# Performance work log

Hardware: AMD Instinct MI355X
Metric: run time of the kernel (lower is better)

The kernel has to match this reference:

```python
import jax, jax.numpy as jnp
import numpy as np

B, S, F_IN, D, DFF, MEM, L, H = 32, 512, 64, 512, 2048, 1024, 3, 8
K_NEIGH = 3
TEMP = 1.0


def _pos_encoding(s, d):
    pos = np.arange(s, dtype=np.float64)[:, None]
    div = np.exp(np.arange(0, d, 2, dtype=np.float64) * (-np.log(10000.0) / d))
    pe = np.zeros((s, d), np.float32)
    pe[:, 0::2] = np.sin(pos * div)
    pe[:, 1::2] = np.cos(pos * div)
    return jnp.asarray(pe)


def _ln(x, g, b, eps=1e-5):
    m = x.mean(-1, keepdims=True)
    v = ((x - m) ** 2).mean(-1, keepdims=True)
    return (x - m) * jax.lax.rsqrt(v + eps) * g + b


def _mha(x, qkv_w, qkv_b, out_w, out_b):
    b, s, d = x.shape
    dh = d // H
    qkv = x @ qkv_w.T + qkv_b                      # (b,s,3d)
    q, k, v = jnp.split(qkv, 3, axis=-1)
    rs = lambda t: t.reshape(b, s, H, dh).transpose(0, 2, 1, 3)   # (b,h,s,dh)
    q, k, v = rs(q), rs(k), rs(v)
    scores = jnp.einsum('bhqd,bhkd->bhqk', q, k) / np.sqrt(dh).astype(np.float32)
    att = jax.nn.softmax(scores, axis=-1)
    o = jnp.einsum('bhqk,bhkd->bhqd', att, v).transpose(0, 2, 1, 3).reshape(b, s, d)
    return o @ out_w.T + out_b


def _construct_graph(x):
    # x: (B, S, F) -> adjacency (B, F, F) via kNN on rank-1 similarity (as in source)
    f = x.mean(axis=1)                                   # (B,F)
    n = jnp.linalg.norm(f, axis=1, keepdims=True)
    fn = f / jnp.maximum(n, 1e-12)                       # F.normalize over full vector
    sim = jnp.einsum('bi,bj->bij', fn, fn)               # (B,F,F)
    nf = f.shape[1]
    k = min(K_NEIGH, nf - 1)
    _, idx = jax.lax.top_k(sim, k + 1)                   # (B,F,k+1)
    idx = idx[..., 1:]                                   # drop top-1 (self under source's assumption)
    bidx = jnp.arange(f.shape[0])[:, None, None]
    ridx = jnp.arange(nf)[None, :, None]
    A = jnp.zeros((f.shape[0], nf, nf), x.dtype).at[bidx, ridx, idx].set(1.0)
    A = jnp.maximum(A, jnp.swapaxes(A, 1, 2))            # symmetrize
    di = jnp.arange(nf)
    return A.at[:, di, di].set(1.0)                      # fill_diagonal_(1)


def _gcn(x, A, w1, b1, w2, b2):
    deg = A.sum(2, keepdims=True)
    An = A / jnp.where(deg == 0, jnp.ones_like(deg), deg)
    xt = jnp.swapaxes(x, 1, 2)                           # (B,F,S)
    h = jax.nn.relu(jnp.einsum('bfg,bgh->bfh', An, xt @ w1.T + b1))
    h = jnp.einsum('bfg,bgh->bfh', An, h @ w2.T + b2)
    return jnp.swapaxes(h, 1, 2)                         # (B,S,F)


def _metg_forward(x, W_in, b_in, qkv_w, qkv_b, out_w, out_b, ln1_g, ln1_b,
                  ln2_g, ln2_b, ff1_w, ff1_b, ff2_w, ff2_b, memory,
                  fc1_w, fc1_b, fc2_w, fc2_b, gc1_w, gc1_b, gc2_w, gc2_b):
    # transformer branch
    h = x @ W_in.T + b_in                                # (B,S,D)
    h = h + _pos_encoding(h.shape[1], h.shape[2])
    for l in range(L):  # post-norm TransformerEncoderLayer, relu FFN, dropout=eval
        h = _ln(h + _mha(h, qkv_w[l], qkv_b[l], out_w[l], out_b[l]), ln1_g[l], ln1_b[l])
        ff = jax.nn.relu(h @ ff1_w[l].T + ff1_b[l]) @ ff2_w[l].T + ff2_b[l]
        h = _ln(h + ff, ln2_g[l], ln2_b[l])
    # memory module
    sims = (h @ memory.T) / TEMP                         # (B,S,MEM)
    attn = jax.nn.softmax(sims, axis=-1)
    upd = attn @ memory                                  # (B,S,D)
    # decoder
    cat = jnp.concatenate([h, upd], axis=-1)             # (B,S,2D)
    t_out = jax.nn.relu(cat @ fc1_w.T + fc1_b) @ fc2_w.T + fc2_b
    # GCN branch
    A = _construct_graph(x)
    g_out = _gcn(x, A, gc1_w, gc1_b, gc2_w, gc2_b)
    return t_out, g_out, attn


def setup_inputs() -> dict:
    key = jax.random.key(0)
    ks = jax.random.split(key, 12)
    w = lambda k, shape, s=0.02: jax.random.normal(k, shape, jnp.float32) * s
    return {
        'x': jax.random.normal(ks[0], (B, S, F_IN), jnp.float32),
        'W_in': w(ks[1], (D, F_IN)), 'b_in': jnp.zeros((D,), jnp.float32),
        'qkv_w': w(ks[2], (L, 3 * D, D)), 'qkv_b': jnp.zeros((L, 3 * D), jnp.float32),
        'out_w': w(ks[3], (L, D, D)), 'out_b': jnp.zeros((L, D), jnp.float32),
        'ln1_g': jnp.ones((L, D), jnp.float32), 'ln1_b': jnp.zeros((L, D), jnp.float32),
        'ln2_g': jnp.ones((L, D), jnp.float32), 'ln2_b': jnp.zeros((L, D), jnp.float32),
        'ff1_w': w(ks[4], (L, DFF, D)), 'ff1_b': jnp.zeros((L, DFF), jnp.float32),
        'ff2_w': w(ks[5], (L, D, DFF)), 'ff2_b': jnp.zeros((L, D), jnp.float32),
        'memory': w(ks[6], (MEM, D), 0.05),
        'fc1_w': w(ks[7], (D, 2 * D)), 'fc1_b': jnp.zeros((D,), jnp.float32),
        'fc2_w': w(ks[8], (F_IN, D)), 'fc2_b': jnp.zeros((F_IN,), jnp.float32),
        'gc1_w': w(ks[9], (D, S)), 'gc1_b': jnp.zeros((D,), jnp.float32),
        'gc2_w': w(ks[10], (S, D)), 'gc2_b': jnp.zeros((S,), jnp.float32),
    }


def reference(x, W_in, b_in, qkv_w, qkv_b, out_w, out_b, ln1_g, ln1_b,
              ln2_g, ln2_b, ff1_w, ff1_b, ff2_w, ff2_b, memory,
              fc1_w, fc1_b, fc2_w, fc2_b, gc1_w, gc1_b, gc2_w, gc2_b):
    return _metg_forward(x, W_in, b_in, qkv_w, qkv_b, out_w, out_b, ln1_g, ln1_b,
                         ln2_g, ln2_b, ff1_w, ff1_b, ff2_w, ff2_b, memory,
                         fc1_w, fc1_b, fc2_w, fc2_b, gc1_w, gc1_b, gc2_w, gc2_b)
```

## Files before the change

### kernel.cpp

```cpp
#include <hip/hip_runtime.h>
#include <hip/hip_bf16.h>
#include <math.h>


namespace {

typedef unsigned short ushort_t;
using bf16x8 = __attribute__((ext_vector_type(8))) __bf16;
using f32x4 = __attribute__((ext_vector_type(4))) float;
using ushort8 = __attribute__((ext_vector_type(8))) unsigned short;

constexpr int Mrows = 32 * 512;

__device__ __forceinline__ unsigned short f2bf(float f) {
  unsigned int u = __builtin_bit_cast(unsigned int, f);
  u += 0x7fffu + ((u >> 16) & 1u);
  return (unsigned short)(u >> 16);
}
__device__ __forceinline__ float bf2f(ushort_t u) {
  unsigned int v = ((unsigned int)u) << 16;
  return __builtin_bit_cast(float, v);
}

__device__ __forceinline__ void g2lds16(const void* g, void* l) {
  __builtin_amdgcn_global_load_lds(
      (const __attribute__((address_space(1))) unsigned int*)g,
      (__attribute__((address_space(3))) unsigned int*)l, 16, 0, 0);
}

template <bool RELU, bool BF16OUT>
__global__ __launch_bounds__(256) void gemm_bf16(const ushort_t* __restrict__ A,
                                                 const ushort_t* __restrict__ B,
                                                 const float* __restrict__ bias,
                                                 void* __restrict__ Cv,
                                                 int M, int N, int K,
                                                 int lda, int ldc) {
  __shared__ __align__(16) ushort_t As[128 * 64];
  __shared__ __align__(16) ushort_t Bs[128 * 64];
  const int t = threadIdx.x;
  const int w = t >> 6, l = t & 63;
  const int m0 = blockIdx.x << 7, n0 = blockIdx.y << 7;
  const int srow = w * 32 + (l >> 3);
  const int scol = ((l & 7) ^ (l >> 3)) << 3;
  const ushort_t* agp = A + (size_t)(m0 + srow) * lda + scol;
  const ushort_t* bgp = B + (size_t)(n0 + srow) * K + scol;
  ushort_t* alds = &As[(w * 32) * 64];
  ushort_t* blds = &Bs[(w * 32) * 64];
  const int wr = w >> 1, wc = w & 1;
  const int lr = l & 15, g = l >> 4;
  const int sw = (l & 7) << 4;
  f32x4 acc[4][4] = {};
  for (int kt = 0; kt < K; kt += 64) {
    __syncthreads();
#pragma unroll
    for (int i = 0; i < 4; ++i) {
      g2lds16(agp + (size_t)(i * 8) * lda + kt, alds + i * 8 * 64);
      g2lds16(bgp + (size_t)(i * 8) * K + kt, blds + i * 8 * 64);
    }
    __syncthreads();
#pragma unroll
    for (int ki = 0; ki < 2; ++ki) {
      bf16x8 af[4], bf[4];
      const int kb = (ki * 64 + g * 16) ^ sw;
#pragma unroll
      for (int mi = 0; mi < 4; ++mi)
        af[mi] = *(const bf16x8*)((const char*)As + (wr * 64 + mi * 16 + lr) * 128 + kb);
#pragma unroll
      for (int ni = 0; ni < 4; ++ni)
        bf[ni] = *(const bf16x8*)((const char*)Bs + (wc * 64 + ni * 16 + lr) * 128 + kb);
#pragma unroll
      for (int mi = 0; mi < 4; ++mi)
#pragma unroll
        for (int ni = 0; ni < 4; ++ni)
          acc[mi][ni] = __builtin_amdgcn_mfma_f32_16x16x32_bf16(af[mi], bf[ni],
                                                                acc[mi][ni], 0, 0, 0);
    }
  }
  float bb[4];
#pragma unroll
  for (int ni = 0; ni < 4; ++ni)
    bb[ni] = bias ? bias[n0 + wc * 64 + ni * 16 + lr] : 0.f;
  const int crow0 = m0 + wr * 64 + g * 4;
  const int ccol0 = n0 + wc * 64 + lr;
  if (!BF16OUT) {
    float* Cf = (float*)Cv;
#pragma unroll
    for (int mi = 0; mi < 4; ++mi)
#pragma unroll
      for (int ni = 0; ni < 4; ++ni)
#pragma unroll
        for (int v = 0; v < 4; ++v) {
          float val = acc[mi][ni][v] + bb[ni];
          if (RELU) val = fmaxf(val, 0.f);
          Cf[(size_t)(crow0 + mi * 16 + v) * ldc + ccol0 + ni * 16] = val;
        }
  } else {
    ushort_t* Cb = (ushort_t*)Cv;
#pragma unroll
    for (int mi = 0; mi < 4; ++mi)
#pragma unroll
      for (int ni = 0; ni < 4; ++ni)
#pragma unroll
        for (int v = 0; v < 4; ++v) {
          float val = acc[mi][ni][v] + bb[ni];
          if (RELU) val = fmaxf(val, 0.f);
          Cb[(size_t)(crow0 + mi * 16 + v) * ldc + ccol0 + ni * 16] = f2bf(val);
        }
  }
}

__global__ __launch_bounds__(256) void flash_attn_mfma(const ushort_t* __restrict__ qkvb,
                                                       ushort_t* __restrict__ ctxb) {
  __shared__ __align__(16) ushort_t Qs[64 * 64];
  __shared__ __align__(16) ushort_t Ks[64 * 64];
  __shared__ __align__(16) ushort_t VT[64 * 64];
  __shared__ __align__(16) ushort_t Ps[64 * 64];
  const int qb = blockIdx.x, hh = blockIdx.y, b = blockIdx.z;
  const int t = threadIdx.x, w = t >> 6, l = t & 63;
  const int g = l >> 4, lr = l & 15, l7 = l & 7;
  const ushort_t* qkv0 = qkvb + (size_t)b * 512 * 1536 + hh * 64;
  {
    const int r8 = l >> 3;
    const int gcol = (l7 ^ r8) << 3;
#pragma unroll
    for (int i = 0; i < 2; ++i) {
      const int row = w * 16 + i * 8 + r8;
      g2lds16(qkv0 + (size_t)(qb * 64 + row) * 1536 + gcol, &Qs[(w * 16 + i * 8) * 64]);
    }
  }
  float mst = -INFINITY, lst = 0.f;
  f32x4 oacc[4] = {};
  const int vk0 = (t & 31) * 2;
  const int vdh0 = (t >> 5) * 8;
  for (int kt = 0; kt < 8; ++kt) {
    __syncthreads();
    {
      const int r8 = l >> 3;
      const int gcol = (l7 ^ r8) << 3;
#pragma unroll
      for (int i = 0; i < 2; ++i) {
        const int row = w * 16 + i * 8 + r8;
        g2lds16(qkv0 + 512 + (size_t)(kt * 64 + row) * 1536 + gcol,
                &Ks[(w * 16 + i * 8) * 64]);
      }
    }
    {
      const ushort_t* vp = qkv0 + 1024 + (size_t)(kt * 64 + vk0) * 1536 + vdh0;
      ushort8 v0 = *(const ushort8*)vp;
      ushort8 v1 = *(const ushort8*)(vp + 1536);
      const int slotbase = vk0 >> 3;
      const int inb = (vk0 & 7) * 2;
#pragma unroll
      for (int e = 0; e < 8; ++e) {
        const int dh = vdh0 + e;
        unsigned int word = (unsigned int)v0[e] | ((unsigned int)v1[e] << 16);
        *(unsigned int*)((char*)VT + dh * 128 + (((slotbase ^ (dh & 7)) << 4) + inb)) = word;
      }
    }
    __syncthreads();
    f32x4 sacc[4] = {};
#pragma unroll
// ... 26 lines not shown
      for (int v = 0; v < 4; ++v) {
        p[mi][v] = __expf(p[mi][v] - mnew);
        csum += p[mi][v];
      }
    csum += __shfl_xor(csum, 16);
    csum += __shfl_xor(csum, 32);
    lst = lst * al + csum;
    mst = mnew;
#pragma unroll
    for (int mi = 0; mi < 4; ++mi) oacc[mi] *= al;
    {
      char* pbase = (char*)Ps + (w * 16 + lr) * 128;
#pragma unroll
      for (int mi = 0; mi < 4; ++mi)
#pragma unroll
        for (int vp2 = 0; vp2 < 2; ++vp2) {
          const int klo = mi * 16 + g * 4 + vp2 * 2;
          unsigned int word = (unsigned int)f2bf(p[mi][vp2 * 2]) |
                              ((unsigned int)f2bf(p[mi][vp2 * 2 + 1]) << 16);
          *(unsigned int*)(pbase + (((klo >> 3) ^ l7) << 4) + (klo & 7) * 2) = word;
        }
    }
#pragma unroll
    for (int ki = 0; ki < 2; ++ki) {
      const int sb = ((ki * 4 + g) ^ l7) << 4;
      bf16x8 pf = *(const bf16x8*)((const char*)Ps + (w * 16 + lr) * 128 + sb);
#pragma unroll
      for (int mi = 0; mi < 4; ++mi) {
        bf16x8 vf = *(const bf16x8*)((const char*)VT + (mi * 16 + lr) * 128 + sb);
        oacc[mi] = __builtin_amdgcn_mfma_f32_16x16x32_bf16(vf, pf, oacc[mi], 0, 0, 0);
      }
    }
  }
  const float inv = 1.f / lst;
  ushort_t* op = ctxb + (size_t)(b * 512 + qb * 64 + w * 16 + lr) * 512 + hh * 64;
#pragma unroll
  for (int mi = 0; mi < 4; ++mi)
#pragma unroll
    for (int vp2 = 0; vp2 < 2; ++vp2) {
      const int dh = mi * 16 + g * 4 + vp2 * 2;
      unsigned int word = (unsigned int)f2bf(oacc[mi][vp2 * 2] * inv) |
                          ((unsigned int)f2bf(oacc[mi][vp2 * 2 + 1] * inv) << 16);
      *(unsigned int*)(op + dh) = word;
    }
}

#define OUTER16(ACC, A4, B4) do { \
  ACC[0][0] += (A4).x*(B4).x; ACC[0][1] += (A4).x*(B4).y; ACC[0][2] += (A4).x*(B4).z; ACC[0][3] += (A4).x*(B4).w; \
  ACC[1][0] += (A4).y*(B4).x; ACC[1][1] += (A4).y*(B4).y; ACC[1][2] += (A4).y*(B4).z; ACC[1][3] += (A4).y*(B4).w; \
  ACC[2][0] += (A4).z*(B4).x; ACC[2][1] += (A4).z*(B4).y; ACC[2][2] += (A4).z*(B4).z; ACC[2][3] += (A4).z*(B4).w; \
  ACC[3][0] += (A4).w*(B4).x; ACC[3][1] += (A4).w*(B4).y; ACC[3][2] += (A4).w*(B4).z; ACC[3][3] += (A4).w*(B4).w; \
} while (0)

template <bool BT, bool RELU, bool PE>
__global__ __launch_bounds__(256) void gemm64(const float* __restrict__ A,
                                              const float* __restrict__ Bm,
                                              const float* __restrict__ bias,
                                              float* __restrict__ C,
                                              int M, int N, int K,
                                              const float* __restrict__ peb,
                                              ushort_t* __restrict__ hbb) {
  __shared__ float As[16][68];
  __shared__ float Bs[16][68];
  const int t = threadIdx.x;
  const int m0 = blockIdx.x << 6;
  const int n0 = blockIdx.y << 6;
  const int r0 = (t >> 4) << 2;
  const int c0 = (t & 15) << 2;
  const int lm = t >> 2;
  const int lk4 = (t & 3) << 2;
  const int lkk = t >> 4;
  const int ln = (t & 15) << 2;
  float acc[4][4] = {{0.f, 0.f, 0.f, 0.f}, {0.f, 0.f, 0.f, 0.f},
                     {0.f, 0.f, 0.f, 0.f}, {0.f, 0.f, 0.f, 0.f}};
  for (int kt = 0; kt < K; kt += 16) {
    __syncthreads();
    float4 av = *reinterpret_cast<const float4*>(A + (size_t)(m0 + lm) * K + kt + lk4);
    As[lk4 + 0][lm] = av.x; As[lk4 + 1][lm] = av.y;
    As[lk4 + 2][lm] = av.z; As[lk4 + 3][lm] = av.w;
    if (BT) {
      float4 bv = *reinterpret_cast<const float4*>(Bm + (size_t)(n0 + lm) * K + kt + lk4);
      Bs[lk4 + 0][lm] = bv.x; Bs[lk4 + 1][lm] = bv.y;
      Bs[lk4 + 2][lm] = bv.z; Bs[lk4 + 3][lm] = bv.w;
    } else {
      float4 bv = *reinterpret_cast<const float4*>(Bm + (size_t)(kt + lkk) * N + n0 + ln);
      *reinterpret_cast<float4*>(&Bs[lkk][ln]) = bv;
    }
    __syncthreads();
#pragma unroll
    for (int k = 0; k < 16; ++k) {
      float4 a4 = *reinterpret_cast<const float4*>(&As[k][r0]);
      float4 b4 = *reinterpret_cast<const float4*>(&Bs[k][c0]);
      OUTER16(acc, a4, b4);
    }
  }
  float bb0 = 0.f, bb1 = 0.f, bb2 = 0.f, bb3 = 0.f;
  if (bias) {
    bb0 = bias[n0 + c0 + 0]; bb1 = bias[n0 + c0 + 1];
    bb2 = bias[n0 + c0 + 2]; bb3 = bias[n0 + c0 + 3];
  }
#pragma unroll
  for (int i = 0; i < 4; ++i) {
    float4 o;
    o.x = acc[i][0] + bb0; o.y = acc[i][1] + bb1;
    o.z = acc[i][2] + bb2; o.w = acc[i][3] + bb3;
    if (RELU) {
      o.x = fmaxf(o.x, 0.f); o.y = fmaxf(o.y, 0.f);
      o.z = fmaxf(o.z, 0.f); o.w = fmaxf(o.w, 0.f);
    }
    const int row = m0 + r0 + i;
    if (PE) {
      float4 p = *reinterpret_cast<const float4*>(peb + (size_t)(row & 511) * 512 + n0 + c0);
      o.x += p.x; o.y += p.y; o.z += p.z; o.w += p.w;
      ushort4 ob;
      ob.x = f2bf(o.x); ob.y = f2bf(o.y); ob.z = f2bf(o.z); ob.w = f2bf(o.w);
      *reinterpret_cast<ushort4*>(hbb + (size_t)row * 512 + n0 + c0) = ob;
    }
    *reinterpret_cast<float4*>(C + (size_t)row * N + n0 + c0) = o;
  }
}

__device__ __forceinline__ float bsum256(float v, float* red) {
#pragma unroll
  for (int off = 32; off; off >>= 1) v += __shfl_down(v, off);
  __syncthreads();
  if ((threadIdx.x & 63) == 0) red[threadIdx.x >> 6] = v;
  __syncthreads();
  return red[0] + red[1] + red[2] + red[3];
}

__device__ __forceinline__ float bmax256(float v, float* red) {
#pragma unroll
  for (int off = 32; off; off >>= 1) v = fmaxf(v, __shfl_down(v, off));
  __syncthreads();
  if ((threadIdx.x & 63) == 0) red[threadIdx.x >> 6] = v;
  __syncthreads();
  return fmaxf(fmaxf(red[0], red[1]), fmaxf(red[2], red[3]));
}

__global__ __launch_bounds__(256) void ln_fused(float* __restrict__ h,
                                                ushort_t* __restrict__ hbo,
                                                int hbs,
                                                const ushort_t* __restrict__ resb,
                                                const float* __restrict__ g,
                                                const float* __restrict__ bt) {
  __shared__ float red[4];
  const size_t row = blockIdx.x;
  float* hp = h + row * 512;
  ushort_t* hbp = hbo + row * hbs;
  const ushort_t* rp = resb + row * 512;
  const int t = threadIdx.x;
  float x0 = hp[t] + bf2f(rp[t]);
  float x1 = hp[t + 256] + bf2f(rp[t + 256]);
  float mean = bsum256(x0 + x1, red) * (1.f / 512.f);
  float d0 = x0 - mean, d1 = x1 - mean;
  float var = bsum256(d0 * d0 + d1 * d1, red) * (1.f / 512.f);
  float rstd = rsqrtf(var + 1e-5f);
  float y0 = d0 * rstd * g[t] + bt[t];
  float y1 = d1 * rstd * g[t + 256] + bt[t + 256];
  hp[t] = y0; hp[t + 256] = y1;
  hbp[t] = f2bf(y0); hbp[t + 256] = f2bf(y1);
}

__global__ __launch_bounds__(256) void softmax1024_cvt(float* __restrict__ p,
                                                       ushort_t* __restrict__ pb) {
  __shared__ float red[4];
  float4* rp = reinterpret_cast<float4*>(p + (size_t)blockIdx.x * 1024);
  ushort4* rb = reinterpret_cast<ushort4*>(pb + (size_t)blockIdx.x * 1024);
  const int t = threadIdx.x;
  float4 v = rp[t];
  float mx = bmax256(fmaxf(fmaxf(v.x, v.y), fmaxf(v.z, v.w)), red);
  float e0 = expf(v.x - mx), e1 = expf(v.y - mx), e2 = expf(v.z - mx), e3 = expf(v.w - mx);
  float sm = bsum256(e0 + e1 + e2 + e3, red);
  float inv = 1.f / sm;
  float4 o = make_float4(e0 * inv, e1 * inv, e2 * inv, e3 * inv);
  rp[t] = o;
  ushort4 ob;
  ob.x = f2bf(o.x); ob.y = f2bf(o.y); ob.z = f2bf(o.z); ob.w = f2bf(o.w);
  rb[t] = ob;
}

__global__ void pe_kernel(float* __restrict__ pe) {
  const int s = blockIdx.x, i = threadIdx.x;
  double div = exp((double)(2 * i) * (-log(10000.0) / 512.0));
  double a = (double)s * div;
  pe[s * 512 + 2 * i] = (float)sin(a);
  pe[s * 512 + 2 * i + 1] = (float)cos(a);
}

__global__ __launch_bounds__(256) void cvt_all(
    const float* __restrict__ qkvw, const float* __restrict__ outw,
    const float* __restrict__ ff1w, const float* __restrict__ ff2w,
    const float* __restrict__ memw, const float* __restrict__ fc1w,
    const float* __restrict__ gc1w, const float* __restrict__ gc2w,
    ushort_t* qkvb, ushort_t* outb, ushort_t* ff1b, ushort_t* ff2b,
    ushort_t* memb, ushort_t* fc1b, ushort_t* gc1b, ushort_t* gc2b) {
  const int gidx = blockIdx.x * 256 + threadIdx.x;
  const float* s; ushort_t* d; int off;
  if (gidx < 589824)        { s = qkvw; d = qkvb; off = gidx; }
  else if (gidx < 786432)   { s = outw; d = outb; off = gidx - 589824; }
  else if (gidx < 1572864)  { s = ff1w; d = ff1b; off = gidx - 786432; }
  else if (gidx < 2359296)  { s = ff2w; d = ff2b; off = gidx - 1572864; }
  else if (gidx < 2490368)  { s = memw; d = memb; off = gidx - 2359296; }
  else if (gidx < 2621440)  { s = fc1w; d = fc1b; off = gidx - 2490368; }
  else if (gidx < 2686976)  { s = gc1w; d = gc1b; off = gidx - 2621440; }
  else                      { s = gc2w; d = gc2b; off = gidx - 2686976; }
  float4 v = reinterpret_cast<const float4*>(s)[off];
  ushort4 o;
  o.x = f2bf(v.x); o.y = f2bf(v.y); o.z = f2bf(v.z); o.w = f2bf(v.w);
  reinterpret_cast<ushort4*>(d)[off] = o;
}

__global__ __launch_bounds__(256) void transpose_cvt(const float* __restrict__ in,
                                                     ushort_t* __restrict__ out) {
  const int g = blockIdx.x * 256 + threadIdx.x;
  const int r = g >> 9, c = g & 511;
  out[(size_t)c * 1024 + r] = f2bf(in[g]);
}

__global__ __launch_bounds__(256) void transpose_x_bf16(const float* __restrict__ x,
                                                        ushort_t* __restrict__ xtb) {
  __shared__ float Ls[64][65];
  const int sc = blockIdx.x, b = blockIdx.y;
  const int t = threadIdx.x;
  const int f = t & 63, sr = t >> 6;
#pragma unroll
  for (int j = 0; j < 16; ++j) {
    const int s = sr + 4 * j;
    Ls[s][f] = x[((size_t)(b * 512 + sc * 64 + s)) * 64 + f];
  }
  __syncthreads();
#pragma unroll
  for (int j = 0; j < 16; ++j) {
    const int fr = sr * 16 + j;
    xtb[((size_t)b * 64 + fr) * 512 + sc * 64 + f] = f2bf(Ls[f][fr]);
  }
}

__global__ __launch_bounds__(256) void fmean2(const float* __restrict__ x,
                                              float* __restrict__ fn) {
  __shared__ float part[4][64];
  const int b = blockIdx.x, t = threadIdx.x;
  const int f = t & 63, sg = t >> 6;
  float acc = 0.f;
  const float* xp = x + ((size_t)b * 512 + sg) * 64 + f;
  for (int s = sg; s < 512; s += 4, xp += 256) acc += *xp;
  part[sg][f] = acc;
  __syncthreads();
  if (t < 64) {
    float m = (part[0][t] + part[1][t] + part[2][t] + part[3][t]) * (1.f / 512.f);
// ... 46 lines not shown
    vals[j0] = v;
    deg += v;
  }
#pragma unroll
  for (int off = 1; off < 4; off <<= 1) deg += __shfl_xor(deg, off);
  const float inv = 1.f / deg;
  float* out = An + ((size_t)b * 64 + i) * 64 + g * 16;
#pragma unroll
  for (int j0 = 0; j0 < 16; ++j0) out[j0] = vals[j0] * inv;
}

template <bool RELU, bool STORE_T>
__global__ __launch_bounds__(256) void bmm_an(const float* __restrict__ An,
                                              const float* __restrict__ X,
                                              float* __restrict__ Y,
                                              ushort_t* __restrict__ Yb) {
  __shared__ float Ag[64][68];
  __shared__ float Xs[64][68];
  const int nc = blockIdx.x << 6;
  const int b = blockIdx.y;
  const int t = threadIdx.x;
  {
    const int i = t >> 2, g0 = (t & 3) << 4;
    const float* ap = An + ((size_t)b * 64 + i) * 64 + g0;
#pragma unroll
    for (int j = 0; j < 16; ++j) Ag[g0 + j][i] = ap[j];
  }
  {
    const int g = t >> 2, n4 = (t & 3) << 4;
    const float* xp = X + ((size_t)b * 64 + g) * 512 + nc + n4;
#pragma unroll
    for (int j = 0; j < 4; ++j)
      *reinterpret_cast<float4*>(&Xs[g][n4 + 4 * j]) =
          *reinterpret_cast<const float4*>(xp + 4 * j);
  }
  __syncthreads();
  const int r0 = (t >> 4) << 2, c0 = (t & 15) << 2;
  float acc[4][4] = {{0.f, 0.f, 0.f, 0.f}, {0.f, 0.f, 0.f, 0.f},
                     {0.f, 0.f, 0.f, 0.f}, {0.f, 0.f, 0.f, 0.f}};
#pragma unroll 8
  for (int g = 0; g < 64; ++g) {
    float4 a4 = *reinterpret_cast<const float4*>(&Ag[g][r0]);
    float4 x4 = *reinterpret_cast<const float4*>(&Xs[g][c0]);
    OUTER16(acc, a4, x4);
  }
  if (!STORE_T) {
#pragma unroll
    for (int i = 0; i < 4; ++i) {
      float4 o = make_float4(acc[i][0], acc[i][1], acc[i][2], acc[i][3]);
      if (RELU) {
        o.x = fmaxf(o.x, 0.f); o.y = fmaxf(o.y, 0.f);
        o.z = fmaxf(o.z, 0.f); o.w = fmaxf(o.w, 0.f);
      }
      *reinterpret_cast<float4*>(Y + ((size_t)b * 64 + r0 + i) * 512 + nc + c0) = o;
      if (RELU && Yb) {
        ushort4 ob;
        ob.x = f2bf(o.x); ob.y = f2bf(o.y); ob.z = f2bf(o.z); ob.w = f2bf(o.w);
        *reinterpret_cast<ushort4*>(Yb + ((size_t)b * 64 + r0 + i) * 512 + nc + c0) = ob;
      }
    }
  } else {
#pragma unroll
    for (int j = 0; j < 4; ++j) {
      float4 o = make_float4(acc[0][j], acc[1][j], acc[2][j], acc[3][j]);
      *reinterpret_cast<float4*>(Y + ((size_t)b * 512 + nc + c0 + j) * 64 + r0) = o;
    }
  }
}

}

extern "C" void kernel_launch(void* const* d_in, const int* in_sizes, int n_in,
                              void* d_out, int out_size, void* d_ws, size_t ws_size,
                              hipStream_t stream) {
  const float* x     = (const float*)d_in[0];
  const float* W_in  = (const float*)d_in[1];
  const float* b_in  = (const float*)d_in[2];
  const float* qkv_w = (const float*)d_in[3];
  const float* qkv_b = (const float*)d_in[4];
  const float* out_w = (const float*)d_in[5];
  const float* out_b = (const float*)d_in[6];
  const float* ln1_g = (const float*)d_in[7];
  const float* ln1_b = (const float*)d_in[8];
  const float* ln2_g = (const float*)d_in[9];
  const float* ln2_b = (const float*)d_in[10];
  const float* ff1_w = (const float*)d_in[11];
  const float* ff1_b = (const float*)d_in[12];
  const float* ff2_w = (const float*)d_in[13];
  const float* ff2_b = (const float*)d_in[14];
  const float* memw  = (const float*)d_in[15];
  const float* fc1_w = (const float*)d_in[16];
  const float* fc1_b = (const float*)d_in[17];
  const float* fc2_w = (const float*)d_in[18];
  const float* fc2_b = (const float*)d_in[19];
  const float* gc1_w = (const float*)d_in[20];
  const float* gc1_b = (const float*)d_in[21];
  const float* gc2_w = (const float*)d_in[22];
  const float* gc2_b = (const float*)d_in[23];

  char* wsb = (char*)d_ws;
  float*    h      = (float*)(wsb + 0);
  ushort_t* hb     = (ushort_t*)(wsb + 33554432);
  char*     U1     = wsb + 50331648;
  ushort_t* ctxb   = (ushort_t*)(wsb + 150994944);
  ushort_t* resb   = (ushort_t*)(wsb + 167772160);
  float*    pe     = (float*)(wsb + 184549376);
  ushort_t* qkv_wb = (ushort_t*)(wsb + 185597952);
  ushort_t* out_wb = (ushort_t*)(wsb + 190316544);
  ushort_t* ff1_wb = (ushort_t*)(wsb + 191889408);
  ushort_t* ff2_wb = (ushort_t*)(wsb + 198180864);
  ushort_t* mem_b  = (ushort_t*)(wsb + 204472320);
  ushort_t* memT_b = (ushort_t*)(wsb + 205520896);
  ushort_t* fc1_wb = (ushort_t*)(wsb + 206569472);
  ushort_t* gc1_wb = (ushort_t*)(wsb + 207618048);
  ushort_t* gc2_wb = (ushort_t*)(wsb + 208142336);
  float*    fn     = (float*)(wsb + 208666624);
  float*    An     = (float*)(wsb + 208674816);

  ushort_t* qkvb  = (ushort_t*)U1;
  ushort_t* midb  = (ushort_t*)U1;
  ushort_t* attnb = (ushort_t*)U1;
  ushort_t* catb  = (ushort_t*)(U1 + 33554432);
  float*    bufC  = (float*)U1;
  ushort_t* xtb   = (ushort_t*)U1;
  float*    t1    = (float*)(U1 + 2097152);
  float*    h1    = (float*)(U1 + 6291456);
  ushort_t* h1b   = (ushort_t*)(U1 + 10485760);
  float*    t2    = (float*)(U1 + 12582912);

  float* t_out = (float*)d_out;
  float* g_out = t_out + 1048576;
  float* attn  = g_out + 1048576;

  hipLaunchKernelGGL(cvt_all, dim3(10752), dim3(256), 0, stream,
                     qkv_w, out_w, ff1_w, ff2_w, memw, fc1_w, gc1_w, gc2_w,
                     qkv_wb, out_wb, ff1_wb, ff2_wb, mem_b, fc1_wb, gc1_wb, gc2_wb);
  hipLaunchKernelGGL(transpose_cvt, dim3(2048), dim3(256), 0, stream, memw, memT_b);
  hipLaunchKernelGGL(pe_kernel, dim3(512), dim3(256), 0, stream, pe);

  hipLaunchKernelGGL((gemm64<true, false, true>), dim3(256, 8), dim3(256), 0, stream,
                     x, W_in, b_in, h, Mrows, 512, 64, pe, hb);

  for (int l = 0; l < 3; ++l) {
    hipLaunchKernelGGL((gemm_bf16<false, true>), dim3(128, 12), dim3(256), 0, stream,
                       hb, qkv_wb + (size_t)l * 786432, qkv_b + l * 1536, qkvb,
                       Mrows, 1536, 512, 512, 1536);
    hipLaunchKernelGGL(flash_attn_mfma, dim3(8, 8, 32), dim3(256), 0, stream, qkvb, ctxb);
    hipLaunchKernelGGL((gemm_bf16<false, true>), dim3(128, 4), dim3(256), 0, stream,
                       ctxb, out_wb + (size_t)l * 262144, out_b + l * 512, resb,
                       Mrows, 512, 512, 512, 512);
    hipLaunchKernelGGL(ln_fused, dim3(Mrows), dim3(256), 0, stream,
                       h, hb, 512, resb, ln1_g + l * 512, ln1_b + l * 512);
    hipLaunchKernelGGL((gemm_bf16<true, true>), dim3(128, 16), dim3(256), 0, stream,
                       hb, ff1_wb + (size_t)l * 1048576, ff1_b + l * 2048, midb,
                       Mrows, 2048, 512, 512, 2048);
    hipLaunchKernelGGL((gemm_bf16<false, true>), dim3(128, 4), dim3(256), 0, stream,
                       midb, ff2_wb + (size_t)l * 1048576, ff2_b + l * 512, resb,
                       Mrows, 512, 2048, 2048, 512);
    if (l < 2) {
      hipLaunchKernelGGL(ln_fused, dim3(Mrows), dim3(256), 0, stream,
                         h, hb, 512, resb, ln2_g + l * 512, ln2_b + l * 512);
    } else {
      hipLaunchKernelGGL(ln_fused, dim3(Mrows), dim3(256), 0, stream,
                         h, catb, 1024, resb, ln2_g + l * 512, ln2_b + l * 512);
    }
  }

  hipLaunchKernelGGL((gemm_bf16<false, false>), dim3(128, 8), dim3(256), 0, stream,
                     catb, mem_b, (const float*)nullptr, attn,
                     Mrows, 1024, 512, 1024, 1024);
  hipLaunchKernelGGL(softmax1024_cvt, dim3(Mrows), dim3(256), 0, stream, attn, attnb);
  hipLaunchKernelGGL((gemm_bf16<false, true>), dim3(128, 4), dim3(256), 0, stream,
                     attnb, memT_b, (const float*)nullptr, catb + 512,
                     Mrows, 512, 1024, 1024, 1024);
  hipLaunchKernelGGL((gemm_bf16<true, false>), dim3(128, 4), dim3(256), 0, stream,
                     catb, fc1_wb, fc1_b, bufC, Mrows, 512, 1024, 1024, 512);
  hipLaunchKernelGGL((gemm64<true, false, false>), dim3(256, 1), dim3(256), 0, stream,
                     bufC, fc2_w, fc2_b, t_out, Mrows, 64, 512,
                     (const float*)nullptr, (ushort_t*)nullptr);

  hipLaunchKernelGGL(fmean2, dim3(32), dim3(256), 0, stream, x, fn);
  hipLaunchKernelGGL(graph_kernel2, dim3(32), dim3(256), 0, stream, fn, An);
  hipLaunchKernelGGL(transpose_x_bf16, dim3(8, 32), dim3(256), 0, stream, x, xtb);
  hipLaunchKernelGGL((gemm_bf16<false, false>), dim3(16, 4), dim3(256), 0, stream,
                     xtb, gc1_wb, gc1_b, t1, 2048, 512, 512, 512, 512);
  hipLaunchKernelGGL((bmm_an<true, false>), dim3(8, 32), dim3(256), 0, stream,
                     An, t1, h1, h1b);
  hipLaunchKernelGGL((gemm_bf16<false, false>), dim3(16, 4), dim3(256), 0, stream,
                     h1b, gc2_wb, gc2_b, t2, 2048, 512, 512, 512, 512);
  hipLaunchKernelGGL((bmm_an<false, true>), dim3(8, 32), dim3(256), 0, stream,
                     An, t2, g_out, (ushort_t*)nullptr);
}
```

Before: 971.7 us.

## Widen bf16 GEMM tiles to 128x256, drop fp32 residual stream, wave-per-row LN/softmax

```diff
diff --git a/kernel.cpp b/kernel.cpp
--- a/kernel.cpp
+++ b/kernel.cpp
@@ -11,6 +11,7 @@
 using ushort8 = __attribute__((ext_vector_type(8))) unsigned short;
 
 constexpr int Mrows = 32 * 512;
+constexpr size_t MB = 1048576;
 
 __device__ __forceinline__ unsigned short f2bf(float f) {
   unsigned int u = __builtin_bit_cast(unsigned int, f);
@@ -33,80 +34,76 @@
                                                  const ushort_t* __restrict__ B,
                                                  const float* __restrict__ bias,
                                                  void* __restrict__ Cv,
-                                                 int M, int N, int K,
-                                                 int lda, int ldc) {
+                                                 int K, int lda, int ldc, int Nclip) {
   __shared__ __align__(16) ushort_t As[128 * 64];
-  __shared__ __align__(16) ushort_t Bs[128 * 64];
+  __shared__ __align__(16) ushort_t Bs[256 * 64];
   const int t = threadIdx.x;
   const int w = t >> 6, l = t & 63;
-  const int m0 = blockIdx.x << 7, n0 = blockIdx.y << 7;
-  const int srow = w * 32 + (l >> 3);
-  const int scol = ((l & 7) ^ (l >> 3)) << 3;
-  const ushort_t* agp = A + (size_t)(m0 + srow) * lda + scol;
-  const ushort_t* bgp = B + (size_t)(n0 + srow) * K + scol;
+  const int m0 = blockIdx.x << 7, n0 = blockIdx.y << 8;
+  const int srow8 = l >> 3;
+  const int scol = ((l & 7) ^ srow8) << 3;
+  const ushort_t* agp = A + (size_t)(m0 + w * 32 + srow8) * lda + scol;
+  const ushort_t* bgp = B + (size_t)(n0 + w * 64 + srow8) * K + scol;
   ushort_t* alds = &As[(w * 32) * 64];
-  ushort_t* blds = &Bs[(w * 32) * 64];
+  ushort_t* blds = &Bs[(w * 64) * 64];
   const int wr = w >> 1, wc = w & 1;
   const int lr = l & 15, g = l >> 4;
   const int sw = (l & 7) << 4;
-  f32x4 acc[4][4] = {};
+  f32x4 acc[4][8] = {};
   for (int kt = 0; kt < K; kt += 64) {
     __syncthreads();
 #pragma unroll
-    for (int i = 0; i < 4; ++i) {
+    for (int i = 0; i < 4; ++i)
       g2lds16(agp + (size_t)(i * 8) * lda + kt, alds + i * 8 * 64);
+#pragma unroll
+    for (int i = 0; i < 8; ++i)
       g2lds16(bgp + (size_t)(i * 8) * K + kt, blds + i * 8 * 64);
-    }
     __syncthreads();
 #pragma unroll
     for (int ki = 0; ki < 2; ++ki) {
-      bf16x8 af[4], bf[4];
       const int kb = (ki * 64 + g * 16) ^ sw;
+      bf16x8 af[4];
 #pragma unroll
       for (int mi = 0; mi < 4; ++mi)
         af[mi] = *(const bf16x8*)((const char*)As + (wr * 64 + mi * 16 + lr) * 128 + kb);
 #pragma unroll
-      for (int ni = 0; ni < 4; ++ni)
-        bf[ni] = *(const bf16x8*)((const char*)Bs + (wc * 64 + ni * 16 + lr) * 128 + kb);
-#pragma unroll
-      for (int mi = 0; mi < 4; ++mi)
-#pragma unroll
-        for (int ni = 0; ni < 4; ++ni)
-          acc[mi][ni] = __builtin_amdgcn_mfma_f32_16x16x32_bf16(af[mi], bf[ni],
-                                                                acc[mi][ni], 0, 0, 0);
-    }
-  }
-  float bb[4];
-#pragma unroll
-  for (int ni = 0; ni < 4; ++ni)
-    bb[ni] = bias ? bias[n0 + wc * 64 + ni * 16 + lr] : 0.f;
+      for (int h = 0; h < 2; ++h) {
+        bf16x8 bfh[4];
+#pragma unroll
+        for (int j = 0; j < 4; ++j)
+          bfh[j] = *(const bf16x8*)((const char*)Bs +
+                                    (wc * 128 + (h * 4 + j) * 16 + lr) * 128 + kb);
+#pragma unroll
+        for (int mi = 0; mi < 4; ++mi)
+#pragma unroll
+          for (int j = 0; j < 4; ++j)
+            acc[mi][h * 4 + j] = __builtin_amdgcn_mfma_f32_16x16x32_bf16(
+                af[mi], bfh[j], acc[mi][h * 4 + j], 0, 0, 0);
+      }
+    }
+  }
+  float bb[8];
+#pragma unroll
+  for (int ni = 0; ni < 8; ++ni) {
+    const int ci = n0 + wc * 128 + ni * 16 + lr;
+    bb[ni] = (bias && ci < Nclip) ? bias[ci] : 0.f;
+  }
   const int crow0 = m0 + wr * 64 + g * 4;
-  const int ccol0 = n0 + wc * 64 + lr;
-  if (!BF16OUT) {
-    float* Cf = (float*)Cv;
-#pragma unroll
-    for (int mi = 0; mi < 4; ++mi)
-#pragma unroll
-      for (int ni = 0; ni < 4; ++ni)
-#pragma unroll
-        for (int v = 0; v < 4; ++v) {
-          float val = acc[mi][ni][v] + bb[ni];
-          if (RELU) val = fmaxf(val, 0.f);
-          Cf[(size_t)(crow0 + mi * 16 + v) * ldc + ccol0 + ni * 16] = val;
-        }
-  } else {
-    ushort_t* Cb = (ushort_t*)Cv;
-#pragma unroll
-    for (int mi = 0; mi < 4; ++mi)
-#pragma unroll
-      for (int ni = 0; ni < 4; ++ni)
-#pragma unroll
-        for (int v = 0; v < 4; ++v) {
-          float val = acc[mi][ni][v] + bb[ni];
-          if (RELU) val = fmaxf(val, 0.f);
-          Cb[(size_t)(crow0 + mi * 16 + v) * ldc + ccol0 + ni * 16] = f2bf(val);
-        }
-  }
+#pragma unroll
+  for (int mi = 0; mi < 4; ++mi)
+#pragma unroll
+    for (int ni = 0; ni < 8; ++ni) {
+      const int ci = n0 + wc * 128 + ni * 16 + lr;
+      if (ci >= Nclip) continue;
+#pragma unroll
+      for (int v = 0; v < 4; ++v) {
+        float val = acc[mi][ni][v] + bb[ni];
+        if (RELU) val = fmaxf(val, 0.f);
+        const size_t off = (size_t)(crow0 + mi * 16 + v) * ldc + ci;
+        if (BF16OUT) ((ushort_t*)Cv)[off] = f2bf(val);
+        else         ((float*)Cv)[off] = val;
+      }
+    }
 }
 
 __global__ __launch_bounds__(256) void flash_attn_mfma(const ushort_t* __restrict__ qkvb,
@@ -239,14 +236,11 @@
   ACC[3][0] += (A4).w*(B4).x; ACC[3][1] += (A4).w*(B4).y; ACC[3][2] += (A4).w*(B4).z; ACC[3][3] += (A4).w*(B4).w; \
 } while (0)
 
-template <bool BT, bool RELU, bool PE>
-__global__ __launch_bounds__(256) void gemm64(const float* __restrict__ A,
-                                              const float* __restrict__ Bm,
-                                              const float* __restrict__ bias,
-                                              float* __restrict__ C,
-                                              int M, int N, int K,
-                                              const float* __restrict__ peb,
-                                              ushort_t* __restrict__ hbb) {
+__global__ __launch_bounds__(256) void win_pe_gemm(const float* __restrict__ A,
+                                                   const float* __restrict__ Bm,
+                                                   const float* __restrict__ bias,
+                                                   const float* __restrict__ peb,
+                                                   ushort_t* __restrict__ hbb) {
   __shared__ float As[16][68];
   __shared__ float Bs[16][68];
   const int t = threadIdx.x;
@@ -256,23 +250,16 @@
   const int c0 = (t & 15) << 2;
   const int lm = t >> 2;
   const int lk4 = (t & 3) << 2;
-  const int lkk = t >> 4;
-  const int ln = (t & 15) << 2;
   float acc[4][4] = {{0.f, 0.f, 0.f, 0.f}, {0.f, 0.f, 0.f, 0.f},
                      {0.f, 0.f, 0.f, 0.f}, {0.f, 0.f, 0.f, 0.f}};
-  for (int kt = 0; kt < K; kt += 16) {
+  for (int kt = 0; kt < 64; kt += 16) {
     __syncthreads();
-    float4 av = *reinterpret_cast<const float4*>(A + (size_t)(m0 + lm) * K + kt + lk4);
+    float4 av = *reinterpret_cast<const float4*>(A + (size_t)(m0 + lm) * 64 + kt + lk4);
     As[lk4 + 0][lm] = av.x; As[lk4 + 1][lm] = av.y;
     As[lk4 + 2][lm] = av.z; As[lk4 + 3][lm] = av.w;
-    if (BT) {
-      float4 bv = *reinterpret_cast<const float4*>(Bm + (size_t)(n0 + lm) * K + kt + lk4);
-      Bs[lk4 + 0][lm] = bv.x; Bs[lk4 + 1][lm] = bv.y;
-      Bs[lk4 + 2][lm] = bv.z; Bs[lk4 + 3][lm] = bv.w;
-    } else {
-      float4 bv = *reinterpret_cast<const float4*>(Bm + (size_t)(kt + lkk) * N + n0 + ln);
-      *reinterpret_cast<float4*>(&Bs[lkk][ln]) = bv;
-    }
+    float4 bv = *reinterpret_cast<const float4*>(Bm + (size_t)(n0 + lm) * 64 + kt + lk4);
+    Bs[lk4 + 0][lm] = bv.x; Bs[lk4 + 1][lm] = bv.y;
+    Bs[lk4 + 2][lm] = bv.z; Bs[lk4 + 3][lm] = bv.w;
     __syncthreads();
 #pragma unroll
     for (int k = 0; k < 16; ++k) {
@@ -281,90 +268,92 @@
       OUTER16(acc, a4, b4);
     }
   }
-  float bb0 = 0.f, bb1 = 0.f, bb2 = 0.f, bb3 = 0.f;
-  if (bias) {
-    bb0 = bias[n0 + c0 + 0]; bb1 = bias[n0 + c0 + 1];
-    bb2 = bias[n0 + c0 + 2]; bb3 = bias[n0 + c0 + 3];
-  }
+  const float bb0 = bias[n0 + c0 + 0], bb1 = bias[n0 + c0 + 1];
+  const float bb2 = bias[n0 + c0 + 2], bb3 = bias[n0 + c0 + 3];
 #pragma unroll
   for (int i = 0; i < 4; ++i) {
-    float4 o;
-    o.x = acc[i][0] + bb0; o.y = acc[i][1] + bb1;
-    o.z = acc[i][2] + bb2; o.w = acc[i][3] + bb3;
-    if (RELU) {
-      o.x = fmaxf(o.x, 0.f); o.y = fmaxf(o.y, 0.f);
-      o.z = fmaxf(o.z, 0.f); o.w = fmaxf(o.w, 0.f);
-    }
     const int row = m0 + r0 + i;
-    if (PE) {
-      float4 p = *reinterpret_cast<const float4*>(peb + (size_t)(row & 511) * 512 + n0 + c0);
-      o.x += p.x; o.y += p.y; o.z += p.z; o.w += p.w;
-      ushort4 ob;
-      ob.x = f2bf(o.x); ob.y = f2bf(o.y); ob.z = f2bf(o.z); ob.w = f2bf(o.w);
-      *reinterpret_cast<ushort4*>(hbb + (size_t)row * 512 + n0 + c0) = ob;
-    }
-    *reinterpret_cast<float4*>(C + (size_t)row * N + n0 + c0) = o;
-  }
-}
-
-__device__ __forceinline__ float bsum256(float v, float* red) {
-#pragma unroll
-  for (int off = 32; off; off >>= 1) v += __shfl_down(v, off);
-  __syncthreads();
-  if ((threadIdx.x & 63) == 0) red[threadIdx.x >> 6] = v;
-  __syncthreads();
-  return red[0] + red[1] + red[2] + red[3];
-}
-
-__device__ __forceinline__ float bmax256(float v, float* red) {
-#pragma unroll
-  for (int off = 32; off; off >>= 1) v = fmaxf(v, __shfl_down(v, off));
-  __syncthreads();
-  if ((threadIdx.x & 63) == 0) red[threadIdx.x >> 6] = v;
-  __syncthreads();
-  return fmaxf(fmaxf(red[0], red[1]), fmaxf(red[2], red[3]));
-}
-
-__global__ __launch_bounds__(256) void ln_fused(float* __restrict__ h,
-                                                ushort_t* __restrict__ hbo,
-                                                int hbs,
-                                                const ushort_t* __restrict__ resb,
-                                                const float* __restrict__ g,
-                                                const float* __restrict__ bt) {
-  __shared__ float red[4];
-  const size_t row = blockIdx.x;
-  float* hp = h + row * 512;
-  ushort_t* hbp = hbo + row * hbs;
-  const ushort_t* rp = resb + row * 512;
+    float4 p = *reinterpret_cast<const float4*>(peb + (size_t)(row & 511) * 512 + n0 + c0);
+    ushort4 ob;
+    ob.x = f2bf(acc[i][0] + bb0 + p.x);
+    ob.y = f2bf(acc[i][1] + bb1 + p.y);
+    ob.z = f2bf(acc[i][2] + bb2 + p.z);
+    ob.w = f2bf(acc[i][3] + bb3 + p.w);
+    *reinterpret_cast<ushort4*>(hbb + (size_t)row * 512 + n0 + c0) = ob;
+  }
+}
+
+__global__ __launch_bounds__(256) void ln_wave(const ushort_t* __restrict__ hbi,
+                                               const ushort_t* __restrict__ resb,
+                                               const float* __restrict__ g,
+                                               const float* __restrict__ bt,
+                                               ushort_t* __restrict__ hbo, int hbs) {
   const int t = threadIdx.x;
-  float x0 = hp[t] + bf2f(rp[t]);
-  float x1 = hp[t + 256] + bf2f(rp[t + 256]);
-  float mean = bsum256(x0 + x1, red) * (1.f / 512.f);
-  float d0 = x0 - mean, d1 = x1 - mean;
-  float var = bsum256(d0 * d0 + d1 * d1, red) * (1.f / 512.f);
-  float rstd = rsqrtf(var + 1e-5f);
-  float y0 = d0 * rstd * g[t] + bt[t];
-  float y1 = d1 * rstd * g[t + 256] + bt[t + 256];
-  hp[t] = y0; hp[t + 256] = y1;
-  hbp[t] = f2bf(y0); hbp[t + 256] = f2bf(y1);
-}
-
-__global__ __launch_bounds__(256) void softmax1024_cvt(float* __restrict__ p,
-                                                       ushort_t* __restrict__ pb) {
-  __shared__ float red[4];
-  float4* rp = reinterpret_cast<float4*>(p + (size_t)blockIdx.x * 1024);
-  ushort4* rb = reinterpret_cast<ushort4*>(pb + (size_t)blockIdx.x * 1024);
+  const size_t row = (size_t)blockIdx.x * 4 + (t >> 6);
+  const int lane = t & 63;
+  const size_t base = row * 512 + lane * 8;
+  ushort8 hv = *reinterpret_cast<const ushort8*>(hbi + base);
+  ushort8 rv = *reinterpret_cast<const ushort8*>(resb + base);
+  float xs[8];
+  float sum = 0.f;
+#pragma unroll
+  for (int i = 0; i < 8; ++i) { xs[i] = bf2f(hv[i]) + bf2f(rv[i]); sum += xs[i]; }
+#pragma unroll
+  for (int off = 1; off < 64; off <<= 1) sum += __shfl_xor(sum, off);
+  const float mean = sum * (1.f / 512.f);
+  float vs = 0.f;
+#pragma unroll
+  for (int i = 0; i < 8; ++i) { xs[i] -= mean; vs += xs[i] * xs[i]; }
+#pragma unroll
+  for (int off = 1; off < 64; off <<= 1) vs += __shfl_xor(vs, off);
+  const float rstd = rsqrtf(vs * (1.f / 512.f) + 1e-5f);
+  float4 g0 = *reinterpret_cast<const float4*>(g + lane * 8);
+  float4 g1 = *reinterpret_cast<const float4*>(g + lane * 8 + 4);
+  float4 b0 = *reinterpret_cast<const float4*>(bt + lane * 8);
+  float4 b1 = *reinterpret_cast<const float4*>(bt + lane * 8 + 4);
+  ushort8 o;
+  o[0] = f2bf(xs[0] * rstd * g0.x + b0.x); o[1] = f2bf(xs[1] * rstd * g0.y + b0.y);
+  o[2] = f2bf(xs[2] * rstd * g0.z + b0.z); o[3] = f2bf(xs[3] * rstd * g0.w + b0.w);
+  o[4] = f2bf(xs[4] * rstd * g1.x + b1.x); o[5] = f2bf(xs[5] * rstd * g1.y + b1.y);
+  o[6] = f2bf(xs[6] * rstd * g1.z + b1.z); o[7] = f2bf(xs[7] * rstd * g1.w + b1.w);
+  *reinterpret_cast<ushort8*>(hbo + row * hbs + lane * 8) = o;
+}
+
+__global__ __launch_bounds__(256) void softmax_wave(const ushort_t* __restrict__ simsb,
+                                                    float* __restrict__ attn,
+                                                    ushort_t* __restrict__ attnb) {
   const int t = threadIdx.x;
-  float4 v = rp[t];
-  float mx = bmax256(fmaxf(fmaxf(v.x, v.y), fmaxf(v.z, v.w)), red);
-  float e0 = expf(v.x - mx), e1 = expf(v.y - mx), e2 = expf(v.z - mx), e3 = expf(v.w - mx);
-  float sm = bsum256(e0 + e1 + e2 + e3, red);
-  float inv = 1.f / sm;
-  float4 o = make_float4(e0 * inv, e1 * inv, e2 * inv, e3 * inv);
-  rp[t] = o;
-  ushort4 ob;
-  ob.x = f2bf(o.x); ob.y = f2bf(o.y); ob.z = f2bf(o.z); ob.w = f2bf(o.w);
-  rb[t] = ob;
+  const size_t row = (size_t)blockIdx.x * 4 + (t >> 6);
+  const int lane = t & 63;
+  const size_t base = row * 1024 + lane * 16;
+  ushort8 v0 = *reinterpret_cast<const ushort8*>(simsb + base);
+  ushort8 v1 = *reinterpret_cast<const ushort8*>(simsb + base + 8);
+  float xs[16];
+  float mx = -INFINITY;
+#pragma unroll
+  for (int i = 0; i < 8; ++i) { xs[i] = bf2f(v0[i]); xs[i + 8] = bf2f(v1[i]); }
+#pragma unroll
+  for (int i = 0; i < 16; ++i) mx = fmaxf(mx, xs[i]);
+#pragma unroll
+  for (int off = 1; off < 64; off <<= 1) mx = fmaxf(mx, __shfl_xor(mx, off));
+  float sum = 0.f;
+#pragma unroll
+  for (int i = 0; i < 16; ++i) { xs[i] = __expf(xs[i] - mx); sum += xs[i]; }
+#pragma unroll
+  for (int off = 1; off < 64; off <<= 1) sum += __shfl_xor(sum, off);
+  const float inv = 1.f / sum;
+  ushort8 o0, o1;
+#pragma unroll
+  for (int i = 0; i < 16; ++i) xs[i] *= inv;
+#pragma unroll
+  for (int i = 0; i < 4; ++i) {
+    float4 f = make_float4(xs[4 * i], xs[4 * i + 1], xs[4 * i + 2], xs[4 * i + 3]);
+    *reinterpret_cast<float4*>(attn + base + 4 * i) = f;
+  }
+#pragma unroll
+  for (int i = 0; i < 8; ++i) { o0[i] = f2bf(xs[i]); o1[i] = f2bf(xs[i + 8]); }
+  *reinterpret_cast<ushort8*>(attnb + base) = o0;
+  *reinterpret_cast<ushort8*>(attnb + base + 8) = o1;
 }
 
 __global__ void pe_kernel(float* __restrict__ pe) {
@@ -380,9 +369,22 @@
     const float* __restrict__ ff1w, const float* __restrict__ ff2w,
     const float* __restrict__ memw, const float* __restrict__ fc1w,
     const float* __restrict__ gc1w, const float* __restrict__ gc2w,
+    const float* __restrict__ fc2w,
     ushort_t* qkvb, ushort_t* outb, ushort_t* ff1b, ushort_t* ff2b,
-    ushort_t* memb, ushort_t* fc1b, ushort_t* gc1b, ushort_t* gc2b) {
+    ushort_t* memb, ushort_t* fc1b, ushort_t* gc1b, ushort_t* gc2b,
+    ushort_t* fc2p) {
   const int gidx = blockIdx.x * 256 + threadIdx.x;
+  if (gidx >= 2785280) return;
+  if (gidx >= 2752512) {
+    const int off = gidx - 2752512;
+    ushort4 o = {0, 0, 0, 0};
+    if (off < 8192) {
+      float4 v = reinterpret_cast<const float4*>(fc2w)[off];
+      o.x = f2bf(v.x); o.y = f2bf(v.y); o.z = f2bf(v.z); o.w = f2bf(v.w);
+    }
+    reinterpret_cast<ushort4*>(fc2p)[off] = o;
+    return;
+  }
   const float* s; ushort_t* d; int off;
   if (gidx < 589824)        { s = qkvw; d = qkvb; off = gidx; }
   else if (gidx < 786432)   { s = outw; d = outb; off = gidx - 589824; }
@@ -535,12 +537,9 @@
         o.x = fmaxf(o.x, 0.f); o.y = fmaxf(o.y, 0.f);
         o.z = fmaxf(o.z, 0.f); o.w = fmaxf(o.w, 0.f);
       }
-      *reinterpret_cast<float4*>(Y + ((size_t)b * 64 + r0 + i) * 512 + nc + c0) = o;
-      if (RELU && Yb) {
-        ushort4 ob;
-        ob.x = f2bf(o.x); ob.y = f2bf(o.y); ob.z = f2bf(o.z); ob.w = f2bf(o.w);
-        *reinterpret_cast<ushort4*>(Yb + ((size_t)b * 64 + r0 + i) * 512 + nc + c0) = ob;
-      }
+      ushort4 ob;
+      ob.x = f2bf(o.x); ob.y = f2bf(o.y); ob.z = f2bf(o.z); ob.w = f2bf(o.w);
+      *reinterpret_cast<ushort4*>(Yb + ((size_t)b * 64 + r0 + i) * 512 + nc + c0) = ob;
     }
   } else {
 #pragma unroll
@@ -582,95 +581,96 @@
   const float* gc2_b = (const float*)d_in[23];
 
   char* wsb = (char*)d_ws;
-  float*    h      = (float*)(wsb + 0);
-  ushort_t* hb     = (ushort_t*)(wsb + 33554432);
-  char*     U1     = wsb + 50331648;
-  ushort_t* ctxb   = (ushort_t*)(wsb + 150994944);
-  ushort_t* resb   = (ushort_t*)(wsb + 167772160);
-  float*    pe     = (float*)(wsb + 184549376);
-  ushort_t* qkv_wb = (ushort_t*)(wsb + 185597952);
-  ushort_t* out_wb = (ushort_t*)(wsb + 190316544);
-  ushort_t* ff1_wb = (ushort_t*)(wsb + 191889408);
-  ushort_t* ff2_wb = (ushort_t*)(wsb + 198180864);
-  ushort_t* mem_b  = (ushort_t*)(wsb + 204472320);
-  ushort_t* memT_b = (ushort_t*)(wsb + 205520896);
-  ushort_t* fc1_wb = (ushort_t*)(wsb + 206569472);
-  ushort_t* gc1_wb = (ushort_t*)(wsb + 207618048);
-  ushort_t* gc2_wb = (ushort_t*)(wsb + 208142336);
-  float*    fn     = (float*)(wsb + 208666624);
-  float*    An     = (float*)(wsb + 208674816);
-
-  ushort_t* qkvb  = (ushort_t*)U1;
-  ushort_t* midb  = (ushort_t*)U1;
-  ushort_t* attnb = (ushort_t*)U1;
-  ushort_t* catb  = (ushort_t*)(U1 + 33554432);
-  float*    bufC  = (float*)U1;
-  ushort_t* xtb   = (ushort_t*)U1;
-  float*    t1    = (float*)(U1 + 2097152);
-  float*    h1    = (float*)(U1 + 6291456);
-  ushort_t* h1b   = (ushort_t*)(U1 + 10485760);
-  float*    t2    = (float*)(U1 + 12582912);
+  ushort_t* hb     = (ushort_t*)(wsb + 0);
+  ushort_t* ctxb   = (ushort_t*)(wsb + 16 * MB);
+  ushort_t* resb   = (ushort_t*)(wsb + 32 * MB);
+  char*     U1     = wsb + 48 * MB;
+  float*    pe     = (float*)(wsb + 144 * MB);
+  ushort_t* qkv_wb = (ushort_t*)(wsb + 146 * MB);
+  ushort_t* out_wb = (ushort_t*)(wsb + 151 * MB);
+  ushort_t* ff1_wb = (ushort_t*)(wsb + 153 * MB);
+  ushort_t* ff2_wb = (ushort_t*)(wsb + 160 * MB);
+  ushort_t* mem_b  = (ushort_t*)(wsb + 166 * MB);
+  ushort_t* memT_b = (ushort_t*)(wsb + 167 * MB);
+  ushort_t* fc1_wb = (ushort_t*)(wsb + 168 * MB);
+  ushort_t* gc1_wb = (ushort_t*)(wsb + 169 * MB);
+  ushort_t* gc2_wb = (ushort_t*)(wsb + 169 * MB + 524288);
+  ushort_t* fc2_wp = (ushort_t*)(wsb + 170 * MB);
+  float*    fn     = (float*)(wsb + 171 * MB);
+  float*    An     = (float*)(wsb + 172 * MB);
+
+  ushort_t* qkvb    = (ushort_t*)U1;
+  ushort_t* midb    = (ushort_t*)U1;
+  ushort_t* catb    = (ushort_t*)U1;
+  ushort_t* simsb   = (ushort_t*)(U1 + 32 * MB);
+  ushort_t* attnb   = (ushort_t*)(U1 + 64 * MB);
+  ushort_t* fc1outb = (ushort_t*)(U1 + 64 * MB);
+  ushort_t* xtb  = (ushort_t*)U1;
+  float*    t1   = (float*)(U1 + 2 * MB);
+  ushort_t* h1b  = (ushort_t*)(U1 + 6 * MB);
+  float*    t2   = (float*)(U1 + 8 * MB);
 
   float* t_out = (float*)d_out;
   float* g_out = t_out + 1048576;
   float* attn  = g_out + 1048576;
 
-  hipLaunchKernelGGL(cvt_all, dim3(10752), dim3(256), 0, stream,
-                     qkv_w, out_w, ff1_w, ff2_w, memw, fc1_w, gc1_w, gc2_w,
-                     qkv_wb, out_wb, ff1_wb, ff2_wb, mem_b, fc1_wb, gc1_wb, gc2_wb);
+  hipLaunchKernelGGL(cvt_all, dim3(10880), dim3(256), 0, stream,
+                     qkv_w, out_w, ff1_w, ff2_w, memw, fc1_w, gc1_w, gc2_w, fc2_w,
+                     qkv_wb, out_wb, ff1_wb, ff2_wb, mem_b, fc1_wb, gc1_wb, gc2_wb,
+                     fc2_wp);
   hipLaunchKernelGGL(transpose_cvt, dim3(2048), dim3(256), 0, stream, memw, memT_b);
   hipLaunchKernelGGL(pe_kernel, dim3(512), dim3(256), 0, stream, pe);
 
-  hipLaunchKernelGGL((gemm64<true, false, true>), dim3(256, 8), dim3(256), 0, stream,
-                     x, W_in, b_in, h, Mrows, 512, 64, pe, hb);
+  hipLaunchKernelGGL(win_pe_gemm, dim3(256, 8), dim3(256), 0, stream,
+                     x, W_in, b_in, pe, hb);
 
   for (int l = 0; l < 3; ++l) {
-    hipLaunchKernelGGL((gemm_bf16<false, true>), dim3(128, 12), dim3(256), 0, stream,
+    hipLaunchKernelGGL((gemm_bf16<false, true>), dim3(128, 6), dim3(256), 0, stream,
                        hb, qkv_wb + (size_t)l * 786432, qkv_b + l * 1536, qkvb,
-                       Mrows, 1536, 512, 512, 1536);
+                       512, 512, 1536, 1536);
     hipLaunchKernelGGL(flash_attn_mfma, dim3(8, 8, 32), dim3(256), 0, stream, qkvb, ctxb);
-    hipLaunchKernelGGL((gemm_bf16<false, true>), dim3(128, 4), dim3(256), 0, stream,
+    hipLaunchKernelGGL((gemm_bf16<false, true>), dim3(128, 2), dim3(256), 0, stream,
                        ctxb, out_wb + (size_t)l * 262144, out_b + l * 512, resb,
-                       Mrows, 512, 512, 512, 512);
-    hipLaunchKernelGGL(ln_fused, dim3(Mrows), dim3(256), 0, stream,
-                       h, hb, 512, resb, ln1_g + l * 512, ln1_b + l * 512);
-    hipLaunchKernelGGL((gemm_bf16<true, true>), dim3(128, 16), dim3(256), 0, stream,
+                       512, 512, 512, 512);
+    hipLaunchKernelGGL(ln_wave, dim3(Mrows / 4), dim3(256), 0, stream,
+                       hb, resb, ln1_g + l * 512, ln1_b + l * 512, hb, 512);
+    hipLaunchKernelGGL((gemm_bf16<true, true>), dim3(128, 8), dim3(256), 0, stream,
                        hb, ff1_wb + (size_t)l * 1048576, ff1_b + l * 2048, midb,
-                       Mrows, 2048, 512, 512, 2048);
-    hipLaunchKernelGGL((gemm_bf16<false, true>), dim3(128, 4), dim3(256), 0, stream,
+                       512, 512, 2048, 2048);
+    hipLaunchKernelGGL((gemm_bf16<false, true>), dim3(128, 2), dim3(256), 0, stream,
                        midb, ff2_wb + (size_t)l * 1048576, ff2_b + l * 512, resb,
-                       Mrows, 512, 2048, 2048, 512);
+                       2048, 2048, 512, 512);
     if (l < 2) {
-      hipLaunchKernelGGL(ln_fused, dim3(Mrows), dim3(256), 0, stream,
-                         h, hb, 512, resb, ln2_g + l * 512, ln2_b + l * 512);
+      hipLaunchKernelGGL(ln_wave, dim3(Mrows / 4), dim3(256), 0, stream,
+                         hb, resb, ln2_g + l * 512, ln2_b + l * 512, hb, 512);
     } else {
-      hipLaunchKernelGGL(ln_fused, dim3(Mrows), dim3(256), 0, stream,
-                         h, catb, 1024, resb, ln2_g + l * 512, ln2_b + l * 512);
-    }
-  }
-
-  hipLaunchKernelGGL((gemm_bf16<false, false>), dim3(128, 8), dim3(256), 0, stream,
-                     catb, mem_b, (const float*)nullptr, attn,
-                     Mrows, 1024, 512, 1024, 1024);
-  hipLaunchKernelGGL(softmax1024_cvt, dim3(Mrows), dim3(256), 0, stream, attn, attnb);
+      hipLaunchKernelGGL(ln_wave, dim3(Mrows / 4), dim3(256), 0, stream,
+                         hb, resb, ln2_g + l * 512, ln2_b + l * 512, catb, 1024);
+    }
+  }
+
   hipLaunchKernelGGL((gemm_bf16<false, true>), dim3(128, 4), dim3(256), 0, stream,
+                     catb, mem_b, (const float*)nullptr, simsb,
+                     512, 1024, 1024, 1024);
+  hipLaunchKernelGGL(softmax_wave, dim3(Mrows / 4), dim3(256), 0, stream,
+                     simsb, attn, attnb);
+  hipLaunchKernelGGL((gemm_bf16<false, true>), dim3(128, 2), dim3(256), 0, stream,
                      attnb, memT_b, (const float*)nullptr, catb + 512,
-                     Mrows, 512, 1024, 1024, 1024);
-  hipLaunchKernelGGL((gemm_bf16<true, false>), dim3(128, 4), dim3(256), 0, stream,
-                     catb, fc1_wb, fc1_b, bufC, Mrows, 512, 1024, 1024, 512);
-  hipLaunchKernelGGL((gemm64<true, false, false>), dim3(256, 1), dim3(256), 0, stream,
-                     bufC, fc2_w, fc2_b, t_out, Mrows, 64, 512,
-                     (const float*)nullptr, (ushort_t*)nullptr);
+                     1024, 1024, 1024, 512);
+  hipLaunchKernelGGL((gemm_bf16<true, true>), dim3(128, 2), dim3(256), 0, stream,
+                     catb, fc1_wb, fc1_b, fc1outb, 1024, 1024, 512, 512);
+  hipLaunchKernelGGL((gemm_bf16<false, false>), dim3(128, 1), dim3(256), 0, stream,
+                     fc1outb, fc2_wp, fc2_b, t_out, 512, 512, 64, 64);
 
   hipLaunchKernelGGL(fmean2, dim3(32), dim3(256), 0, stream, x, fn);
   hipLaunchKernelGGL(graph_kernel2, dim3(32), dim3(256), 0, stream, fn, An);
   hipLaunchKernelGGL(transpose_x_bf16, dim3(8, 32), dim3(256), 0, stream, x, xtb);
-  hipLaunchKernelGGL((gemm_bf16<false, false>), dim3(16, 4), dim3(256), 0, stream,
-                     xtb, gc1_wb, gc1_b, t1, 2048, 512, 512, 512, 512);
+  hipLaunchKernelGGL((gemm_bf16<false, false>), dim3(16, 2), dim3(256), 0, stream,
+                     xtb, gc1_wb, gc1_b, t1, 512, 512, 512, 512);
   hipLaunchKernelGGL((bmm_an<true, false>), dim3(8, 32), dim3(256), 0, stream,
-                     An, t1, h1, h1b);
-  hipLaunchKernelGGL((gemm_bf16<false, false>), dim3(16, 4), dim3(256), 0, stream,
-                     h1b, gc2_wb, gc2_b, t2, 2048, 512, 512, 512, 512);
+                     An, t1, (float*)nullptr, h1b);
+  hipLaunchKernelGGL((gemm_bf16<false, false>), dim3(16, 2), dim3(256), 0, stream,
+                     h1b, gc2_wb, gc2_b, t2, 512, 512, 512, 512);
   hipLaunchKernelGGL((bmm_an<false, true>), dim3(8, 32), dim3(256), 0, stream,
                      An, t2, g_out, (ushort_t*)nullptr);
 }
```

Result: slower. 1.237 ms (+27.3%).
